# Performance work log

Hardware: AMD Instinct MI355X
Metric: run time of the kernel (lower is better)

## Reference

```python
import jax, jax.numpy as jnp
import numpy as np

N_HEAD = 16
SPARSE_TOPK = 64
NEG_INF = float('-inf')


def setup_inputs() -> dict:
    key = jax.random.key(0)
    ks = jax.random.split(key, 12)
    B, T, C = 4, 1024, 1024
    s = 0.02
    q = jax.random.normal(ks[0], (B, T, C), jnp.float32)
    kv = jax.random.normal(ks[1], (B, T, C), jnp.float32)  # forward asserts k == v
    tgt_mask = jnp.tril(jnp.ones((T, T), jnp.bool_)).reshape(1, 1, T, T)
    inp = {'q': q, 'k': kv, 'v': kv, 'tgt_mask': tgt_mask}
    for i, n in enumerate(['Wq', 'Wk', 'Wv', 'Wo']):
        inp[n] = jax.random.normal(ks[2 + i], (C, C), jnp.float32) * s
    for i, n in enumerate(['bq', 'bk', 'bv', 'bo']):
        inp[n] = jax.random.normal(ks[6 + i], (C,), jnp.float32) * s
    return inp


def reference(q, k, v, tgt_mask, Wq, Wk, Wv, Wo, bq, bk, bv, bo):
    B, T, C = q.shape
    H = N_HEAD
    hd = C // H
    scale = 1.0 / np.sqrt(hd).astype(np.float32)
    # QKV projections -> [B, H, T, hd]
    qh = (q @ Wq + bq).reshape(B, T, H, hd).transpose(0, 2, 1, 3)
    kh = (k @ Wk + bk).reshape(B, T, H, hd).transpose(0, 2, 1, 3)
    vh = (v @ Wv + bv).reshape(B, T, H, hd).transpose(0, 2, 1, 3)
    # full attention scores [B, H, T, T]
    att = jnp.einsum('bhtd,bhsd->bhts', qh, kh) * scale
    # causal mask: masked_fill where tgt_mask == 0
    att = jnp.where(tgt_mask[:, :, :T, :T], att, NEG_INF)
    # top-k sparse pruning: keep entries >= k-th largest per row (ties kept)
    top, _ = jax.lax.top_k(att, SPARSE_TOPK)
    vk = top[..., -1:]  # [B, H, T, 1]
    att = jnp.where(att < vk, NEG_INF, att)
    att = jax.nn.softmax(att, axis=-1)
    # dropout is identity in eval (p=0.0)
    y = jnp.einsum('bhts,bhsd->bhtd', att, vh)
    y = y.transpose(0, 2, 1, 3).reshape(B, T, C)
    return y @ Wo + bo
```

## Files before the change

kernel.cpp:

```cpp
#include <hip/hip_runtime.h>
#include <hip/hip_bf16.h>
#include <math.h>

typedef __attribute__((ext_vector_type(8))) short short8;
typedef __attribute__((ext_vector_type(4))) float f32x4;
typedef __attribute__((ext_vector_type(4))) int int4v;

#define LOG2E 1.4426950408889634f

static __device__ __forceinline__ unsigned short f2bf(float f) {
  unsigned u = __float_as_uint(f);
  u = u + 0x7FFFu + ((u >> 16) & 1u);
  return (unsigned short)(u >> 16);
}

static __device__ __forceinline__ unsigned keyof(float x) {
  unsigned u = __float_as_uint(x);
  return (u & 0x80000000u) ? ~u : (u | 0x80000000u);
}
static __device__ __forceinline__ float keyinv(unsigned k) {
  unsigned u = (k & 0x80000000u) ? (k & 0x7FFFFFFFu) : ~k;
  return __uint_as_float(u);
}

static __device__ __forceinline__ void gld_lds16(const unsigned short* g, unsigned short* l) {
  __builtin_amdgcn_global_load_lds(
      (const __attribute__((address_space(1))) void*)g,
      (__attribute__((address_space(3))) void*)l, 16, 0, 0);
}

__global__ __launch_bounds__(256) void cvt3_k(const float* __restrict__ q,
                                              const float* __restrict__ k,
                                              const float* __restrict__ v,
                                              unsigned short* __restrict__ oq,
                                              unsigned short* __restrict__ ok,
                                              unsigned short* __restrict__ ov) {
  const int y = blockIdx.y;
  const float* in = (y == 0) ? q : (y == 1) ? k : v;
  unsigned short* out = (y == 0) ? oq : (y == 1) ? ok : ov;
  const int i = blockIdx.x * 256 + threadIdx.x;
  const f32x4* p = (const f32x4*)in + 2 * (size_t)i;
  f32x4 a = p[0], b = p[1];
  short8 r;
  r[0] = (short)f2bf(a[0]); r[1] = (short)f2bf(a[1]);
  r[2] = (short)f2bf(a[2]); r[3] = (short)f2bf(a[3]);
  r[4] = (short)f2bf(b[0]); r[5] = (short)f2bf(b[1]);
  r[6] = (short)f2bf(b[2]); r[7] = (short)f2bf(b[3]);
  ((short8*)out)[i] = r;
}

__global__ __launch_bounds__(256) void wtrans4_k(const float* __restrict__ Wq,
                                                 const float* __restrict__ Wk,
                                                 const float* __restrict__ Wv,
                                                 const float* __restrict__ Wo,
                                                 unsigned short* __restrict__ Wqt,
                                                 unsigned short* __restrict__ Wkt,
                                                 unsigned short* __restrict__ Wvt,
                                                 unsigned short* __restrict__ Wot) {
  const int z = blockIdx.z;
  const float* W = (z == 0) ? Wq : (z == 1) ? Wk : (z == 2) ? Wv : Wo;
  unsigned short* Wt = (z == 0) ? Wqt : (z == 1) ? Wkt : (z == 2) ? Wvt : Wot;
  __shared__ float tile[32][33];
  const int tx = threadIdx.x, ty = threadIdx.y;
  const int x0 = blockIdx.x * 32, y0 = blockIdx.y * 32;
#pragma unroll
  for (int j = 0; j < 4; ++j)
    tile[ty + j * 8][tx] = W[(y0 + ty + j * 8) * 1024 + x0 + tx];
  __syncthreads();
#pragma unroll
  for (int j = 0; j < 4; ++j)
    Wt[(x0 + ty + j * 8) * 1024 + (y0 + tx)] = f2bf(tile[tx][ty + j * 8]);
}

template <int MODE>
static __device__ __forceinline__ void gemm_body(unsigned short* As, unsigned short* Bs,
                                                 const unsigned short* __restrict__ A,
                                                 const unsigned short* __restrict__ Bt,
                                                 const float* __restrict__ bias,
                                                 void* __restrict__ out) {
  const int tid = threadIdx.x;
  const int lane = tid & 63, w = tid >> 6;
  const int wr = w >> 1, wc = w & 1;
  const int m0 = blockIdx.y * 128, n0 = blockIdx.x * 128;
  const int l15 = lane & 15, l4 = lane >> 4;
  f32x4 acc[4][4] = {};
  const int r0 = tid >> 2, s0 = (tid & 3) * 8;
  const int r1 = r0 + 64;
  const unsigned short* gA0 = A + (m0 + r0) * 1024 + s0;
  const unsigned short* gA1 = A + (m0 + r1) * 1024 + s0;
  const unsigned short* gB0 = Bt + (n0 + r0) * 1024 + s0;
  const unsigned short* gB1 = Bt + (n0 + r1) * 1024 + s0;
  unsigned short* lA0 = As + r0 * 32 + s0;
  unsigned short* lA1 = As + r1 * 32 + s0;
  unsigned short* lB0 = Bs + r0 * 32 + s0;
  unsigned short* lB1 = Bs + r1 * 32 + s0;

  for (int kt = 0; kt < 32; ++kt) {
    const int k0 = kt * 32;
    __syncthreads();
    gld_lds16(gA0 + k0, lA0);
    gld_lds16(gA1 + k0, lA1);
    gld_lds16(gB0 + k0, lB0);
    gld_lds16(gB1 + k0, lB1);
    __syncthreads();
    short8 af[4], bfr[4];
#pragma unroll
    for (int i = 0; i < 4; ++i) {
      af[i]  = *(const short8*)(As + (wr * 64 + i * 16 + l15) * 32 + l4 * 8);
      bfr[i] = *(const short8*)(Bs + (wc * 64 + i * 16 + l15) * 32 + l4 * 8);
    }
#pragma unroll
    for (int i = 0; i < 4; ++i)
#pragma unroll
      for (int j = 0; j < 4; ++j)
        acc[i][j] = __builtin_amdgcn_mfma_f32_16x16x32_bf16(af[i], bfr[j], acc[i][j], 0, 0, 0);
  }
#pragma unroll
  for (int i = 0; i < 4; ++i) {
#pragma unroll
    for (int j = 0; j < 4; ++j) {
      const int n = n0 + wc * 64 + j * 16 + l15;
      const float bv = bias[n];
#pragma unroll
      for (int r = 0; r < 4; ++r) {
        const int m = m0 + wr * 64 + i * 16 + l4 * 4 + r;
        const float v = acc[i][j][r] + bv;
        if (MODE == 2) {
          ((float*)out)[m * 1024 + n] = v;
        } else {
          const int bb = m >> 10, t = m & 1023, hh = n >> 6, dd = n & 63;
          const unsigned short bfv = f2bf(v);
          if (MODE == 0)
            ((unsigned short*)out)[(((bb << 4) + hh) * 1024 + t) * 64 + dd] = bfv;
          else
            ((unsigned short*)out)[(((bb << 4) + hh) * 64 + dd) * 1024 + t] = bfv;
        }
      }
    }
  }
}

__global__ __launch_bounds__(256) void gemm_qkv_k(
    const unsigned short* qbf, const unsigned short* kbf, const unsigned short* vbf,
    const unsigned short* Wqt, const unsigned short* Wkt, const unsigned short* Wvt,
    const float* bq, const float* bk, const float* bv,
    unsigned short* Qh, unsigned short* Kh, unsigned short* Vth) {
  __shared__ unsigned short As[128 * 32], Bs[128 * 32];
  const int z = blockIdx.z;
  const unsigned short* A  = (z == 0) ? qbf : ((z == 1) ? kbf : vbf);
  const unsigned short* Bt = (z == 0) ? Wqt : ((z == 1) ? Wkt : Wvt);
  const float* bias        = (z == 0) ? bq  : ((z == 1) ? bk  : bv);
  if (z == 2) gemm_body<1>(As, Bs, A, Bt, bias, Vth);
  else        gemm_body<0>(As, Bs, A, Bt, bias, z ? Kh : Qh);
}

__global__ __launch_bounds__(256) void gemm_out_k(const unsigned short* Y,
                                                  const unsigned short* Wot,
                                                  const float* bo, float* out) {
  __shared__ unsigned short As[128 * 32], Bs[128 * 32];
  gemm_body<2>(As, Bs, Y, Wot, bo, out);
}

__global__ __launch_bounds__(512, 8) void attn_k(const unsigned short* __restrict__ Q,
                                                 const unsigned short* __restrict__ K,
                                                 const unsigned short* __restrict__ Vt,
                                                 unsigned short* __restrict__ Y) {
  extern __shared__ __align__(16) char smem[];
  const int tid = threadIdx.x, lane = tid & 63, w = tid >> 6;
  const int t0 = (63 - blockIdx.x) * 16;
  const int h = blockIdx.y, b = blockIdx.z;
  const unsigned short* Qp = Q + (((b * 16 + h) * 1024) + t0) * 64;
  const unsigned short* Kh = K + (b * 16 + h) * 65536;
  const unsigned short* Vh = Vt + (b * 16 + h) * 65536;
  const int L = t0 + 16;
  const int Lpad = (L + 31) & ~31;
  const int nCT = L >> 4;
  const int l15 = lane & 15, l4 = lane >> 4;
  float* RED = (float*)(smem + 32768);

#define SADDR(r, cc) (((((r) << 9) + (cc)) << 2) ^ (((r) & 7) << 4))
#define SREF(r, cc) (*(float*)(smem + SADDR(r, cc)))
#define PADDR(r, c) ((((r) << 11) + ((c) << 1)) ^ (((r) & 7) << 4))

  const short8 aq0 = *(const short8*)(Qp + l15 * 64 + l4 * 8);
  const short8 aq1 = *(const short8*)(Qp + l15 * 64 + 32 + l4 * 8);

  auto qk_chunk = [&](int tlo, int thi) {
    for (int ct = tlo + w; ct < thi; ct += 8) {
      const int c0 = ct * 16;
      const short8 kb0 = *(const short8*)(Kh + (c0 + l15) * 64 + l4 * 8);
      const short8 kb1 = *(const short8*)(Kh + (c0 + l15) * 64 + 32 + l4 * 8);
      f32x4 acc = {0.f, 0.f, 0.f, 0.f};
      acc = __builtin_amdgcn_mfma_f32_16x16x32_bf16(aq0, kb0, acc, 0, 0, 0);
      acc = __builtin_amdgcn_mfma_f32_16x16x32_bf16(aq1, kb1, acc, 0, 0, 0);
      const int c = c0 + l15, cc = c & 511;
#pragma unroll
      for (int r = 0; r < 4; ++r) {
        const int row = l4 * 4 + r;
        SREF(row, cc) = (c <= t0 + row) ? acc[r] * 0.125f : -INFINITY;
      }
    }
  };

  qk_chunk(0, (nCT < 32) ? nCT : 32);
  __syncthreads();
  const int rA = w * 2, rB = rA + 1;
  const int LrA = t0 + rA + 1, LrB = t0 + rB + 1;
  float vA[16], vB[16];
#pragma unroll
  for (int i = 0; i < 8; ++i) {
    const int c = lane + (i << 6);
    vA[i] = (c < L) ? SREF(rA, c) : -INFINITY;
    vB[i] = (c < L) ? SREF(rB, c) : -INFINITY;
  }
  if (L > 512) {
    __syncthreads();
    qk_chunk(32, nCT);
    __syncthreads();
#pragma unroll
    for (int i = 8; i < 16; ++i) {
      const int c = 512 + lane + ((i - 8) << 6);
      vA[i] = (c < L) ? SREF(rA, c & 511) : -INFINITY;
      vB[i] = (c < L) ? SREF(rB, c & 511) : -INFINITY;
    }
  } else {
#pragma unroll
    for (int i = 8; i < 16; ++i) { vA[i] = -INFINITY; vB[i] = -INFINITY; }
  }
  __syncthreads();

  float lmA = vA[0], lmB = vB[0];
#pragma unroll
  for (int i = 1; i < 16; ++i) { lmA = fmaxf(lmA, vA[i]); lmB = fmaxf(lmB, vB[i]); }
  float mxA = lmA, mnA = lmA, mxB = lmB, mnB = lmB;
#pragma unroll
  for (int o = 32; o; o >>= 1) {
    mxA = fmaxf(mxA, __shfl_xor(mxA, o));
    mxB = fmaxf(mxB, __shfl_xor(mxB, o));
    mnA = fminf(mnA, __shfl_xor(mnA, o));
    mnB = fminf(mnB, __shfl_xor(mnB, o));
  }

  unsigned loA, hiA, loB, hiB;
  int clA = LrA, chA = 0, clB = LrB, chB = 0;
  if (LrA > 64) {
    loA = (unsigned)__builtin_amdgcn_readfirstlane((int)keyof(mnA));
    hiA = (unsigned)__builtin_amdgcn_readfirstlane((int)keyof(mxA)) + 1u;
  } else { loA = 0u; hiA = 1u; }
  if (LrB > 64) {
    loB = (unsigned)__builtin_amdgcn_readfirstlane((int)keyof(mnB));
    hiB = (unsigned)__builtin_amdgcn_readfirstlane((int)keyof(mxB)) + 1u;
  } else { loB = 0u; hiB = 1u; }

  for (int it = 0; it < 64; ++it) {
    const bool dA = (hiA - loA) > 1u, dB = (hiB - loB) > 1u;
    if (!dA && !dB) break;
    if (dA) {
      const unsigned span = hiA - loA;
      unsigned off;
      if (it & 1) off = span >> 1;
      else {
        const float fr = (float)(clA - 64) / (float)(clA - chA);
        off = (unsigned)(fr * (float)span);
        if (off < 1u) off = 1u;
        if (off > span - 1u) off = span - 1u;
      }
      const unsigned mid = loA + off;
      const float tm = keyinv(mid);
      int cnt = 0;
#pragma unroll
      for (int i = 0; i < 16; ++i) cnt += (int)__popcll(__ballot(vA[i] >= tm));
      if (cnt >= 64) { loA = mid; clA = cnt; if (cnt == 64) hiA = mid + 1u; }
      else { hiA = mid; chA = cnt; }
    }
    if (dB) {
      const unsigned span = hiB - loB;
      unsigned off;
      if (it & 1) off = span >> 1;
      else {
        const float fr = (float)(clB - 64) / (float)(clB - chB);
        off = (unsigned)(fr * (float)span);
        if (off < 1u) off = 1u;
        if (off > span - 1u) off = span - 1u;
      }
      const unsigned mid = loB + off;
      const float tm = keyinv(mid);
      int cnt = 0;
#pragma unroll
      for (int i = 0; i < 16; ++i) cnt += (int)__popcll(__ballot(vB[i] >= tm));
      if (cnt >= 64) { loB = mid; clB = cnt; if (cnt == 64) hiB = mid + 1u; }
      else { hiB = mid; chB = cnt; }
    }
  }
  const float thrA = (LrA > 64) ? keyinv(loA) : -INFINITY;
  const float thrB = (LrB > 64) ? keyinv(loB) : -INFINITY;

  float sA = 0.f, sB = 0.f;
#pragma unroll
  for (int i = 0; i < 16; ++i) {
    const float pA = (vA[i] >= thrA) ? exp2f((vA[i] - mxA) * LOG2E) : 0.f;
    const float pB = (vB[i] >= thrB) ? exp2f((vB[i] - mxB) * LOG2E) : 0.f;
    vA[i] = pA; sA += pA;
    vB[i] = pB; sB += pB;
  }
#pragma unroll
  for (int o = 32; o; o >>= 1) {
    sA += __shfl_xor(sA, o);
    sB += __shfl_xor(sB, o);
  }
  const float invA = 1.f / sA, invB = 1.f / sB;
#pragma unroll
  for (int i = 0; i < 16; ++i) {
    if ((i << 6) < Lpad) {
      const int c = lane + (i << 6);
      *(unsigned short*)(smem + PADDR(rA, c)) = f2bf(vA[i] * invA);
      *(unsigned short*)(smem + PADDR(rB, c)) = f2bf(vB[i] * invB);
    }
  }
  __syncthreads();

  const int nST = Lpad >> 5;
  const int stMid = (nST + 1) >> 1;
  const int d0 = (w & 3) * 16;
  const int stLo = (w < 4) ? 0 : stMid;
  const int stHi = (w < 4) ? stMid : nST;
  f32x4 acc = {0.f, 0.f, 0.f, 0.f};
  for (int st = stLo; st < stHi; ++st) {
    const int sb = st * 32 + l4 * 8;
    const short8 paf = *(const short8*)(smem + PADDR(l15, sb));
    const short8 vb = *(const short8*)(Vh + (d0 + l15) * 1024 + sb);
    acc = __builtin_amdgcn_mfma_f32_16x16x32_bf16(paf, vb, acc, 0, 0, 0);
  }
  if (w >= 4) {
    const int base = (w - 4) * 272 + l15;
#pragma unroll
    for (int r = 0; r < 4; ++r) RED[base + (l4 * 4 + r) * 17] = acc[r];
  }
  __syncthreads();
  if (w < 4) {
    const int base = w * 272 + l15;
    const int d = (h << 6) + d0 + l15;
#pragma unroll
    for (int r = 0; r < 4; ++r) {
      const float vr = acc[r] + RED[base + (l4 * 4 + r) * 17];
      const int tg = t0 + l4 * 4 + r;
      Y[((b << 10) + tg) * 1024 + d] = f2bf(vr);
    }
  }
#undef SADDR
#undef SREF
#undef PADDR
}

extern "C" void kernel_launch(void* const* d_in, const int* in_sizes, int n_in,
                              void* d_out, int out_size, void* d_ws, size_t ws_size,
                              hipStream_t stream) {
  const float* q  = (const float*)d_in[0];
  const float* k  = (const float*)d_in[1];
  const float* v  = (const float*)d_in[2];
  const float* Wq = (const float*)d_in[4];
  const float* Wk = (const float*)d_in[5];
  const float* Wv = (const float*)d_in[6];
  const float* Wo = (const float*)d_in[7];
  const float* bq = (const float*)d_in[8];
  const float* bk = (const float*)d_in[9];
  const float* bv = (const float*)d_in[10];
  const float* bo = (const float*)d_in[11];

  char* ws = (char*)d_ws;
  const size_t MB = 1u << 20;
  unsigned short* qbf = (unsigned short*)(ws + 0 * MB);
  unsigned short* kbf = (unsigned short*)(ws + 8 * MB);
  unsigned short* vbf = (unsigned short*)(ws + 16 * MB);
  unsigned short* Wqt = (unsigned short*)(ws + 24 * MB);
  unsigned short* Wkt = (unsigned short*)(ws + 26 * MB);
  unsigned short* Wvt = (unsigned short*)(ws + 28 * MB);
  unsigned short* Wot = (unsigned short*)(ws + 30 * MB);
  unsigned short* Qh  = (unsigned short*)(ws + 32 * MB);
  unsigned short* Kh  = (unsigned short*)(ws + 40 * MB);
  unsigned short* Vth = (unsigned short*)(ws + 48 * MB);
  unsigned short* Y   = qbf;

  cvt3_k<<<dim3(2048, 3), 256, 0, stream>>>(q, k, v, qbf, kbf, vbf);
  wtrans4_k<<<dim3(32, 32, 4), dim3(32, 8), 0, stream>>>(Wq, Wk, Wv, Wo, Wqt, Wkt, Wvt, Wot);
  gemm_qkv_k<<<dim3(8, 32, 3), 256, 0, stream>>>(qbf, kbf, vbf, Wqt, Wkt, Wvt,
                                                 bq, bk, bv, Qh, Kh, Vth);
  attn_k<<<dim3(64, 16, 4), 512, 37120, stream>>>(Qh, Kh, Vth, Y);
  gemm_out_k<<<dim3(8, 32), 256, 0, stream>>>(Y, Wot, bo, (float*)d_out);
}
```

Before: 222.4 us.

## Specialize attention top-k by row length, vectorize LDS, defer softmax normalization

```diff
diff --git a/kernel.cpp b/kernel.cpp
--- a/kernel.cpp
+++ b/kernel.cpp
@@ -6,7 +6,7 @@
 typedef __attribute__((ext_vector_type(4))) float f32x4;
 typedef __attribute__((ext_vector_type(4))) int int4v;
 
-#define LOG2E 1.4426950408889634f
+#define SCL 0.1803368801111204f
 
 static __device__ __forceinline__ unsigned short f2bf(float f) {
   unsigned u = __float_as_uint(f);
@@ -21,6 +21,13 @@
 static __device__ __forceinline__ float keyinv(unsigned k) {
   unsigned u = (k & 0x80000000u) ? (k & 0x7FFFFFFFu) : ~k;
   return __uint_as_float(u);
+}
+
+static __device__ __forceinline__ int saddr(int r, int cc) {
+  return (((r << 9) + cc) << 2) ^ ((r & 7) << 4);
+}
+static __device__ __forceinline__ int paddr(int r, int c) {
+  return ((r << 11) + (c << 1)) ^ ((r & 7) << 4);
 }
 
 static __device__ __forceinline__ void gld_lds16(const unsigned short* g, unsigned short* l) {
@@ -161,77 +168,14 @@
   gemm_body<2>(As, Bs, Y, Wot, bo, out);
 }
 
-__global__ __launch_bounds__(512, 8) void attn_k(const unsigned short* __restrict__ Q,
-                                                 const unsigned short* __restrict__ K,
-                                                 const unsigned short* __restrict__ Vt,
-                                                 unsigned short* __restrict__ Y) {
-  extern __shared__ __align__(16) char smem[];
-  const int tid = threadIdx.x, lane = tid & 63, w = tid >> 6;
-  const int t0 = (63 - blockIdx.x) * 16;
-  const int h = blockIdx.y, b = blockIdx.z;
-  const unsigned short* Qp = Q + (((b * 16 + h) * 1024) + t0) * 64;
-  const unsigned short* Kh = K + (b * 16 + h) * 65536;
-  const unsigned short* Vh = Vt + (b * 16 + h) * 65536;
-  const int L = t0 + 16;
-  const int Lpad = (L + 31) & ~31;
-  const int nCT = L >> 4;
-  const int l15 = lane & 15, l4 = lane >> 4;
-  float* RED = (float*)(smem + 32768);
-
-#define SADDR(r, cc) (((((r) << 9) + (cc)) << 2) ^ (((r) & 7) << 4))
-#define SREF(r, cc) (*(float*)(smem + SADDR(r, cc)))
-#define PADDR(r, c) ((((r) << 11) + ((c) << 1)) ^ (((r) & 7) << 4))
-
-  const short8 aq0 = *(const short8*)(Qp + l15 * 64 + l4 * 8);
-  const short8 aq1 = *(const short8*)(Qp + l15 * 64 + 32 + l4 * 8);
-
-  auto qk_chunk = [&](int tlo, int thi) {
-    for (int ct = tlo + w; ct < thi; ct += 8) {
-      const int c0 = ct * 16;
-      const short8 kb0 = *(const short8*)(Kh + (c0 + l15) * 64 + l4 * 8);
-      const short8 kb1 = *(const short8*)(Kh + (c0 + l15) * 64 + 32 + l4 * 8);
-      f32x4 acc = {0.f, 0.f, 0.f, 0.f};
-      acc = __builtin_amdgcn_mfma_f32_16x16x32_bf16(aq0, kb0, acc, 0, 0, 0);
-      acc = __builtin_amdgcn_mfma_f32_16x16x32_bf16(aq1, kb1, acc, 0, 0, 0);
-      const int c = c0 + l15, cc = c & 511;
-#pragma unroll
-      for (int r = 0; r < 4; ++r) {
-        const int row = l4 * 4 + r;
-        SREF(row, cc) = (c <= t0 + row) ? acc[r] * 0.125f : -INFINITY;
-      }
-    }
-  };
-
-  qk_chunk(0, (nCT < 32) ? nCT : 32);
-  __syncthreads();
-  const int rA = w * 2, rB = rA + 1;
-  const int LrA = t0 + rA + 1, LrB = t0 + rB + 1;
-  float vA[16], vB[16];
-#pragma unroll
-  for (int i = 0; i < 8; ++i) {
-    const int c = lane + (i << 6);
-    vA[i] = (c < L) ? SREF(rA, c) : -INFINITY;
-    vB[i] = (c < L) ? SREF(rB, c) : -INFINITY;
-  }
-  if (L > 512) {
-    __syncthreads();
-    qk_chunk(32, nCT);
-    __syncthreads();
-#pragma unroll
-    for (int i = 8; i < 16; ++i) {
-      const int c = 512 + lane + ((i - 8) << 6);
-      vA[i] = (c < L) ? SREF(rA, c & 511) : -INFINITY;
-      vB[i] = (c < L) ? SREF(rB, c & 511) : -INFINITY;
-    }
-  } else {
-#pragma unroll
-    for (int i = 8; i < 16; ++i) { vA[i] = -INFINITY; vB[i] = -INFINITY; }
-  }
-  __syncthreads();
-
+template <int NVAL>
+static __device__ __forceinline__ void topk_phase(char* smem, float (&vA)[16], float (&vB)[16],
+                                                  const int lane, const int rA, const int rB,
+                                                  const int LrA, const int LrB, const int Lpad,
+                                                  float* RED2) {
   float lmA = vA[0], lmB = vB[0];
 #pragma unroll
-  for (int i = 1; i < 16; ++i) { lmA = fmaxf(lmA, vA[i]); lmB = fmaxf(lmB, vB[i]); }
+  for (int i = 1; i < NVAL; ++i) { lmA = fmaxf(lmA, vA[i]); lmB = fmaxf(lmB, vB[i]); }
   float mxA = lmA, mnA = lmA, mxB = lmB, mnB = lmB;
 #pragma unroll
   for (int o = 32; o; o >>= 1) {
@@ -269,7 +213,7 @@
       const float tm = keyinv(mid);
       int cnt = 0;
 #pragma unroll
-      for (int i = 0; i < 16; ++i) cnt += (int)__popcll(__ballot(vA[i] >= tm));
+      for (int i = 0; i < NVAL; ++i) cnt += (int)__popcll(__ballot(vA[i] >= tm));
       if (cnt >= 64) { loA = mid; clA = cnt; if (cnt == 64) hiA = mid + 1u; }
       else { hiA = mid; chA = cnt; }
     }
@@ -287,7 +231,7 @@
       const float tm = keyinv(mid);
       int cnt = 0;
 #pragma unroll
-      for (int i = 0; i < 16; ++i) cnt += (int)__popcll(__ballot(vB[i] >= tm));
+      for (int i = 0; i < NVAL; ++i) cnt += (int)__popcll(__ballot(vB[i] >= tm));
       if (cnt >= 64) { loB = mid; clB = cnt; if (cnt == 64) hiB = mid + 1u; }
       else { hiB = mid; chB = cnt; }
     }
@@ -297,25 +241,109 @@
 
   float sA = 0.f, sB = 0.f;
 #pragma unroll
-  for (int i = 0; i < 16; ++i) {
-    const float pA = (vA[i] >= thrA) ? exp2f((vA[i] - mxA) * LOG2E) : 0.f;
-    const float pB = (vB[i] >= thrB) ? exp2f((vB[i] - mxB) * LOG2E) : 0.f;
+  for (int i = 0; i < NVAL; ++i) {
+    const float pA = (vA[i] >= thrA) ? exp2f(vA[i] - mxA) : 0.f;
+    const float pB = (vB[i] >= thrB) ? exp2f(vB[i] - mxB) : 0.f;
     vA[i] = pA; sA += pA;
     vB[i] = pB; sB += pB;
   }
 #pragma unroll
-  for (int o = 32; o; o >>= 1) {
-    sA += __shfl_xor(sA, o);
-    sB += __shfl_xor(sB, o);
-  }
-  const float invA = 1.f / sA, invB = 1.f / sB;
-#pragma unroll
-  for (int i = 0; i < 16; ++i) {
-    if ((i << 6) < Lpad) {
-      const int c = lane + (i << 6);
-      *(unsigned short*)(smem + PADDR(rA, c)) = f2bf(vA[i] * invA);
-      *(unsigned short*)(smem + PADDR(rB, c)) = f2bf(vB[i] * invB);
-    }
+  for (int o = 32; o; o >>= 1) { sA += __shfl_xor(sA, o); sB += __shfl_xor(sB, o); }
+  if (lane == 0) { RED2[rA] = 1.f / sA; RED2[rB] = 1.f / sB; }
+
+#pragma unroll
+  for (int p = 0; p < NVAL / 2; ++p) {
+    const int c = ((p & 3) << 7) + (lane << 1) + ((p >= 4) ? 512 : 0);
+    if (c < Lpad) {
+      const unsigned pkA = (unsigned)f2bf(vA[2 * p]) | ((unsigned)f2bf(vA[2 * p + 1]) << 16);
+      const unsigned pkB = (unsigned)f2bf(vB[2 * p]) | ((unsigned)f2bf(vB[2 * p + 1]) << 16);
+      *(unsigned*)(smem + paddr(rA, c)) = pkA;
+      *(unsigned*)(smem + paddr(rB, c)) = pkB;
+    }
+  }
+}
+
+__global__ __launch_bounds__(512, 6) void attn_k(const unsigned short* __restrict__ Q,
+                                                 const unsigned short* __restrict__ K,
+                                                 const unsigned short* __restrict__ Vt,
+                                                 unsigned short* __restrict__ Y) {
+  extern __shared__ __align__(16) char smem[];
+  const int tid = threadIdx.x, lane = tid & 63, w = tid >> 6;
+  const int t0 = (63 - blockIdx.x) * 16;
+  const int h = blockIdx.y, b = blockIdx.z;
+  const unsigned short* Qp = Q + (((b * 16 + h) * 1024) + t0) * 64;
+  const unsigned short* Kh = K + (b * 16 + h) * 65536;
+  const unsigned short* Vh = Vt + (b * 16 + h) * 65536;
+  const int L = t0 + 16;
+  const int Lpad = (L + 31) & ~31;
+  const int nCT = L >> 4;
+  const int l15 = lane & 15, l4 = lane >> 4;
+  float* RED  = (float*)(smem + 32768);
+  float* RED2 = (float*)(smem + 32768 + 4352);
+
+  const short8 aq0 = *(const short8*)(Qp + l15 * 64 + l4 * 8);
+  const short8 aq1 = *(const short8*)(Qp + l15 * 64 + 32 + l4 * 8);
+
+  auto qk_chunk = [&](int tlo, int thi) {
+    for (int ct = tlo + w; ct < thi; ct += 8) {
+      const int c0 = ct * 16;
+      const short8 kb0 = *(const short8*)(Kh + (c0 + l15) * 64 + l4 * 8);
+      const short8 kb1 = *(const short8*)(Kh + (c0 + l15) * 64 + 32 + l4 * 8);
+      f32x4 acc = {0.f, 0.f, 0.f, 0.f};
+      acc = __builtin_amdgcn_mfma_f32_16x16x32_bf16(aq0, kb0, acc, 0, 0, 0);
+      acc = __builtin_amdgcn_mfma_f32_16x16x32_bf16(aq1, kb1, acc, 0, 0, 0);
+      const int c = c0 + l15, cc = c & 511;
+      if (ct == nCT - 1) {
+#pragma unroll
+        for (int r = 0; r < 4; ++r) {
+          const int row = l4 * 4 + r;
+          *(float*)(smem + saddr(row, cc)) = (c <= t0 + row) ? acc[r] * SCL : -INFINITY;
+        }
+      } else {
+#pragma unroll
+        for (int r = 0; r < 4; ++r)
+          *(float*)(smem + saddr(l4 * 4 + r, cc)) = acc[r] * SCL;
+      }
+    }
+  };
+
+  qk_chunk(0, (nCT < 32) ? nCT : 32);
+  __syncthreads();
+  const int rA = w * 2, rB = rA + 1;
+  const int LrA = t0 + rA + 1, LrB = t0 + rB + 1;
+  float vA[16], vB[16];
+#pragma unroll
+  for (int p = 0; p < 4; ++p) {
+    const int c = (p << 7) + (lane << 1);
+    const float2 tA = *(const float2*)(smem + saddr(rA, c));
+    const float2 tB = *(const float2*)(smem + saddr(rB, c));
+    const bool vld = c < L;
+    vA[2 * p]     = vld ? tA.x : -INFINITY;
+    vA[2 * p + 1] = vld ? tA.y : -INFINITY;
+    vB[2 * p]     = vld ? tB.x : -INFINITY;
+    vB[2 * p + 1] = vld ? tB.y : -INFINITY;
+  }
+  if (L > 512) {
+    __syncthreads();
+    qk_chunk(32, nCT);
+    __syncthreads();
+#pragma unroll
+    for (int p = 0; p < 4; ++p) {
+      const int cc = (p << 7) + (lane << 1);
+      const int cg = 512 + cc;
+      const float2 tA = *(const float2*)(smem + saddr(rA, cc));
+      const float2 tB = *(const float2*)(smem + saddr(rB, cc));
+      const bool vld = cg < L;
+      vA[8 + 2 * p] = vld ? tA.x : -INFINITY;
+      vA[9 + 2 * p] = vld ? tA.y : -INFINITY;
+      vB[8 + 2 * p] = vld ? tB.x : -INFINITY;
+      vB[9 + 2 * p] = vld ? tB.y : -INFINITY;
+    }
+    __syncthreads();
+    topk_phase<16>(smem, vA, vB, lane, rA, rB, LrA, LrB, Lpad, RED2);
+  } else {
+    __syncthreads();
+    topk_phase<8>(smem, vA, vB, lane, rA, rB, LrA, LrB, Lpad, RED2);
   }
   __syncthreads();
 
@@ -327,7 +355,7 @@
   f32x4 acc = {0.f, 0.f, 0.f, 0.f};
   for (int st = stLo; st < stHi; ++st) {
     const int sb = st * 32 + l4 * 8;
-    const short8 paf = *(const short8*)(smem + PADDR(l15, sb));
+    const short8 paf = *(const short8*)(smem + paddr(l15, sb));
     const short8 vb = *(const short8*)(Vh + (d0 + l15) * 1024 + sb);
     acc = __builtin_amdgcn_mfma_f32_16x16x32_bf16(paf, vb, acc, 0, 0, 0);
   }
@@ -342,14 +370,12 @@
     const int d = (h << 6) + d0 + l15;
 #pragma unroll
     for (int r = 0; r < 4; ++r) {
-      const float vr = acc[r] + RED[base + (l4 * 4 + r) * 17];
+      const float inv = RED2[l4 * 4 + r];
+      const float vr = (acc[r] + RED[base + (l4 * 4 + r) * 17]) * inv;
       const int tg = t0 + l4 * 4 + r;
       Y[((b << 10) + tg) * 1024 + d] = f2bf(vr);
     }
   }
-#undef SADDR
-#undef SREF
-#undef PADDR
 }
 
 extern "C" void kernel_launch(void* const* d_in, const int* in_sizes, int n_in,
@@ -385,6 +411,6 @@
   wtrans4_k<<<dim3(32, 32, 4), dim3(32, 8), 0, stream>>>(Wq, Wk, Wv, Wo, Wqt, Wkt, Wvt, Wot);
   gemm_qkv_k<<<dim3(8, 32, 3), 256, 0, stream>>>(qbf, kbf, vbf, Wqt, Wkt, Wvt,
                                                  bq, bk, bv, Qh, Kh, Vth);
-  attn_k<<<dim3(64, 16, 4), 512, 37120, stream>>>(Qh, Kh, Vth, Y);
+  attn_k<<<dim3(64, 16, 4), 512, 37248, stream>>>(Qh, Kh, Vth, Y);
   gemm_out_k<<<dim3(8, 32), 256, 0, stream>>>(Y, Wot, bo, (float*)d_out);
 }
```

After: 250.4 us. +12.6%, slower.
